# Optimization experiments

Hardware: AMD Instinct MI355X
Metric: run time of the kernel (lower is better)

The kernel has to match this reference:

```python
import jax, jax.numpy as jnp
import numpy as np

N = 32          # agents_num
IN_DIM = 16     # node feature dim (excluding 2 pos cols)
HID = 128
HEADS = 4
OUT = 5
DUEL_H = 256
RADIUS = 0.3
LATENT = HID + HID * HEADS * 2  # 1152
BS = 128


def _lin(k, i, o):
    s = 1.0 / np.sqrt(i)
    return jax.random.uniform(k, (i, o), minval=-s, maxval=s, dtype=jnp.float32)


def setup_inputs() -> dict:
    key = jax.random.key(0)
    ks = jax.random.split(key, 16)
    pos = jax.random.uniform(ks[0], (BS, N, 2))
    feats = jax.random.normal(ks[1], (BS, N, IN_DIM))
    aidx = jax.random.randint(ks[2], (BS,), 0, N).astype(jnp.float32)
    node = jnp.concatenate([pos, feats], axis=-1).reshape(BS, N * (2 + IN_DIM))
    obs = jnp.concatenate([node, aidx[:, None]], axis=1)  # (BS, N*(2+IN_DIM)+1)
    return {
        "obs": obs,
        "enc_w1": _lin(ks[3], IN_DIM, HID), "enc_b1": jnp.zeros((HID,)),
        "enc_w2": _lin(ks[4], HID, HID), "enc_b2": jnp.zeros((HID,)),
        "wl1": _lin(ks[5], HID, HEADS * HID), "wr1": _lin(ks[6], HID, HEADS * HID),
        "att1": jax.random.normal(ks[7], (HEADS, HID)) * 0.1, "bias1": jnp.zeros((HEADS * HID,)),
        "wl2": _lin(ks[8], HID * HEADS, HEADS * HID), "wr2": _lin(ks[9], HID * HEADS, HEADS * HID),
        "att2": jax.random.normal(ks[10], (HEADS, HID)) * 0.1, "bias2": jnp.zeros((HEADS * HID,)),
        "q_w1": _lin(ks[11], LATENT, DUEL_H), "q_b1": jnp.zeros((DUEL_H,)),
        "q_w2": _lin(ks[12], DUEL_H, OUT), "q_b2": jnp.zeros((OUT,)),
        "v_w1": _lin(ks[13], LATENT, DUEL_H), "v_b1": jnp.zeros((DUEL_H,)),
        "v_w2": _lin(ks[14], DUEL_H, 1), "v_b2": jnp.zeros((1,)),
    }


def _gatv2(x, adj, wl, wr, att, bias):
    # Dense-masked GATv2 (PyG semantics: lin_l on source j, lin_r on target i,
    # leaky_relu(x_i + x_j) . att, softmax over neighbors j, aggregate lin_l(x_j)).
    bs, n, _ = x.shape
    gl = (x @ wl).reshape(bs, n, HEADS, HID)  # source transform
    gr = (x @ wr).reshape(bs, n, HEADS, HID)  # target transform
    e = jax.nn.leaky_relu(gr[:, :, None] + gl[:, None, :], 0.2)  # [b, i, j, h, c]
    logits = jnp.einsum('bijhc,hc->bijh', e, att)
    logits = jnp.where(adj[..., None], logits, -jnp.inf)  # diag always True (self loops)
    alpha = jax.nn.softmax(logits, axis=2)
    out = jnp.einsum('bijh,bjhc->bihc', alpha, gl).reshape(bs, n, HEADS * HID)
    return out + bias


def reference(obs, enc_w1, enc_b1, enc_w2, enc_b2,
              wl1, wr1, att1, bias1, wl2, wr2, att2, bias2,
              q_w1, q_b1, q_w2, q_b2, v_w1, v_b1, v_w2, v_b2):
    bs = obs.shape[0]
    node = obs[:, :-1].reshape(bs, N, 2 + IN_DIM)
    pos, feats = node[..., :2], node[..., 2:]
    aidx = jnp.clip(obs[:, -1], 0, N - 1).astype(jnp.int32)

    # radius_graph (per-graph, loop=False) + GATv2 add_self_loops => diag True
    d2 = jnp.sum((pos[:, :, None] - pos[:, None, :]) ** 2, axis=-1)  # [bs, N, N]
    adj = (d2 < RADIUS ** 2) | jnp.eye(N, dtype=bool)

    # encoder MLP then ReLU (as in forward)
    h = jax.nn.relu(feats @ enc_w1 + enc_b1)
    x = jax.nn.relu(h @ enc_w2 + enc_b2)  # [bs, N, HID]

    b = jnp.arange(bs)
    x1 = x[b, aidx]  # [bs, HID]

    x = jax.nn.relu(_gatv2(x, adj, wl1, wr1, att1, bias1))  # [bs, N, HID*HEADS]
    x2 = x[b, aidx]

    x = jax.nn.relu(_gatv2(x, adj, wl2, wr2, att2, bias2))
    x3 = x[b, aidx]

    x_cat = jnp.concatenate([x1, x2, x3], axis=1)  # [bs, LATENT]

    q = jax.nn.relu(x_cat @ q_w1 + q_b1) @ q_w2 + q_b2  # [bs, OUT]
    v = jax.nn.relu(x_cat @ v_w1 + v_b1) @ v_w2 + v_b2  # [bs, 1]
    return q - q.mean(axis=1, keepdims=True) + v
```

## Files before the change

### kernel.cpp

```cpp
#include <hip/hip_runtime.h>
#include <hip/hip_bf16.h>

typedef unsigned int uint_t;
typedef unsigned short ushort_t;
typedef __attribute__((ext_vector_type(8))) short short8;
typedef __attribute__((ext_vector_type(4))) float floatx4;

__device__ __forceinline__ float4 fma4(float4 a, float s, float4 w){
  a.x += s*w.x; a.y += s*w.y; a.z += s*w.z; a.w += s*w.w; return a;
}
__device__ __forceinline__ float4 relu4(float4 a){
  return make_float4(fmaxf(a.x,0.f),fmaxf(a.y,0.f),fmaxf(a.z,0.f),fmaxf(a.w,0.f));
}
__device__ __forceinline__ unsigned bf16rne(float f){
  unsigned u = __float_as_uint(f);
  return (u + 0x7fffu + ((u>>16)&1u)) >> 16;
}
__device__ __forceinline__ uint_t packbf(float f){
  unsigned hb = bf16rne(f);
  float hf = __uint_as_float(hb<<16);
  unsigned lb = bf16rne(f - hf);
  return (hb<<16) | lb;
}
__device__ __forceinline__ uint4 pack4(float4 v){
  uint4 u; u.x=packbf(v.x); u.y=packbf(v.y); u.z=packbf(v.z); u.w=packbf(v.w); return u;
}
__device__ __forceinline__ float unpk(uint_t u){
  return __uint_as_float(u & 0xffff0000u) + __uint_as_float(u<<16);
}
#define UNPACK8(u0,u1,hi,lo) \
  hi[0]=(short)(u0.x>>16); lo[0]=(short)u0.x; \
  hi[1]=(short)(u0.y>>16); lo[1]=(short)u0.y; \
  hi[2]=(short)(u0.z>>16); lo[2]=(short)u0.z; \
  hi[3]=(short)(u0.w>>16); lo[3]=(short)u0.w; \
  hi[4]=(short)(u1.x>>16); lo[4]=(short)u1.x; \
  hi[5]=(short)(u1.y>>16); lo[5]=(short)u1.y; \
  hi[6]=(short)(u1.z>>16); lo[6]=(short)u1.z; \
  hi[7]=(short)(u1.w>>16); lo[7]=(short)u1.w;


__global__ __launch_bounds__(256) void prep_kernel(
    const float* __restrict__ obs,
    const float* __restrict__ enc_w1, const float* __restrict__ enc_b1,
    const float* __restrict__ enc_w2, const float* __restrict__ enc_b2,
    const float* __restrict__ wl1, const float* __restrict__ wr1,
    const float* __restrict__ wl2,
    const float* __restrict__ q_w1, const float* __restrict__ v_w1,
    ushort_t* __restrict__ wl1Thi, ushort_t* __restrict__ wl1Tlo,
    ushort_t* __restrict__ wr1Thi, ushort_t* __restrict__ wr1Tlo,
    ushort_t* __restrict__ wl2Thi, ushort_t* __restrict__ wl2Tlo,
    ushort_t* __restrict__ qw1Thi, ushort_t* __restrict__ qw1Tlo,
    ushort_t* __restrict__ vw1Thi, ushort_t* __restrict__ vw1Tlo,
    uint_t* __restrict__ xpk, uint_t* __restrict__ xcatpk,
    unsigned* __restrict__ adjw, int* __restrict__ aiw)
{
  const int t = threadIdx.x, bid = blockIdx.x;
  if (bid >= 512){
    __shared__ float sm[32][33];
    const int cw = bid - 512;
    const float* in; ushort_t* ohi; ushort_t* olo; int K, N, tt;
    if (cw < 64)        { in=wl1;  ohi=wl1Thi; olo=wl1Tlo; K=128;  N=512; tt=cw; }
    else if (cw < 128)  { in=wr1;  ohi=wr1Thi; olo=wr1Tlo; K=128;  N=512; tt=cw-64; }
    else if (cw < 384)  { in=wl2;  ohi=wl2Thi; olo=wl2Tlo; K=512;  N=512; tt=cw-128; }
    else if (cw < 672)  { in=q_w1; ohi=qw1Thi; olo=qw1Tlo; K=1152; N=256; tt=cw-384; }
    else                { in=v_w1; ohi=vw1Thi; olo=vw1Tlo; K=1152; N=256; tt=cw-672; }
    const int ktiles = K>>5;
    const int kt = tt % ktiles, nt = tt / ktiles;
    const int r = t>>5, c = t&31;
    #pragma unroll
    for (int i=0;i<4;i++)
      sm[r+i*8][c] = in[(size_t)(kt*32 + r + i*8)*N + nt*32 + c];
    __syncthreads();
    #pragma unroll
    for (int i=0;i<4;i++){
      const int nl = r + i*8;
      const int n  = nt*32 + nl;
      const float f = sm[c][nl];
      const unsigned hb = bf16rne(f);
      const float hf = __uint_as_float(hb<<16);
      const unsigned lb = bf16rne(f - hf);
      const size_t off = (size_t)(n>>4)*(16*K) + (size_t)kt*512 + (size_t)(n&15)*32 + c;
      ohi[off] = (ushort_t)hb;
      olo[off] = (ushort_t)lb;
    }
    return;
  }
  __shared__ float s_pos[64];
  __shared__ float s_feats[128];
  __shared__ __align__(16) float s_h[8*132];
  __shared__ int s_ai;
  const int s = bid>>2, g = bid&3;
  const float* ob = obs + s*577;

  if (t==0){
    float a = ob[576];
    a = fminf(fmaxf(a, 0.f), 31.f);
    s_ai = (int)a;
    if (g==0) aiw[s] = (int)a;
  }
  if (t < 128){ const int n=t>>4, f=t&15; s_feats[t] = ob[(g*8+n)*18+2+f]; }
  if (g==0 && t>=128 && t<192){ const int u=t-128; s_pos[u] = ob[(u>>1)*18 + (u&1)]; }
  __syncthreads();

  if (g==0 && t < 32){
    const float px = s_pos[2*t], py = s_pos[2*t+1];
    const float R2 = 0.09f;
    unsigned mm = 0u;
    for (int j=0;j<32;j++){
      const float dx = __fsub_rn(px, s_pos[2*j]), dy = __fsub_rn(py, s_pos[2*j+1]);
      const float d2 = __fadd_rn(__fmul_rn(dx,dx), __fmul_rn(dy,dy));
      if (d2 <= R2 || j==t) mm |= (1u<<j);
    }
    adjw[s*32+t] = mm;
  }

  const int n = t>>5, c0 = (t&31)*4;
  {
    float4 a = *(const float4*)(enc_b1+c0);
    #pragma unroll
    for (int f=0; f<16; f++)
      a = fma4(a, s_feats[n*16+f], *(const float4*)(enc_w1 + f*128 + c0));
    *(float4*)&s_h[n*132+c0] = relu4(a);
  }
  __syncthreads();
  {
    float4 a = *(const float4*)(enc_b2+c0);
    for (int k=0;k<128;k+=4){
      const float4 hv = *(const float4*)&s_h[n*132+k];
      a = fma4(a, hv.x, *(const float4*)(enc_w2 + (k+0)*128 + c0));
      a = fma4(a, hv.y, *(const float4*)(enc_w2 + (k+1)*128 + c0));
      a = fma4(a, hv.z, *(const float4*)(enc_w2 + (k+2)*128 + c0));
      a = fma4(a, hv.w, *(const float4*)(enc_w2 + (k+3)*128 + c0));
    }
    a = relu4(a);
    const uint4 p = pack4(a);
    const int i = g*8 + n;
    uint_t* xp = xpk + (size_t)(s*2 + (i>>4))*2048 + (c0>>5)*512 + (i&15)*32 + (c0&31);
    *(uint4*)xp = p;
    if (i == s_ai){
      uint_t* xc = xcatpk + (size_t)(s>>4)*18432 + (c0>>5)*512 + (s&15)*32 + (c0&31);
      *(uint4*)xc = p;
    }
  }
}

__global__ __launch_bounds__(512) void pa1_kernel(
    const uint_t* __restrict__ xpk,
    const ushort_t* __restrict__ wl1Thi, const ushort_t* __restrict__ wl1Tlo,
    const ushort_t* __restrict__ wr1Thi, const ushort_t* __restrict__ wr1Tlo,
    const float* __restrict__ att, const float* __restrict__ bias,
    const unsigned* __restrict__ adjw, const int* __restrict__ aiw,
    uint_t* __restrict__ x2pk, uint_t* __restrict__ xcatpk)
{
  __shared__ __align__(16) float s_gl[32*132];
  __shared__ __align__(16) float s_glB[32*132];
  __shared__ __align__(16) float s_gr[32*132];
  __shared__ __align__(16) float s_grB[32*132];
  __shared__ __align__(16) float s_att[128];
  __shared__ __align__(16) float s_b[128];
  __shared__ float s_lg[32*33];
  __shared__ unsigned s_adj[32];
  const int t = threadIdx.x;
  const int s = blockIdx.x >> 2, h = blockIdx.x & 3;
  const int w = t>>6, lane = t&63, m = lane&15, quad = lane>>4;
  const int ww = w&3, khalf = w>>2;

  if (t < 128){ s_att[t] = att[h*128 + t]; s_b[t] = bias[h*128 + t]; }
  if (t >= 224 && t < 256) s_adj[t-224] = adjw[s*32 + (t-224)];
  const int ai = aiw[s];

  const ushort_t* Bhi = (ww<2) ? wl1Thi : wr1Thi;
  const ushort_t* Blo = (ww<2) ? wl1Tlo : wr1Tlo;
  const int nbase = h*8 + (ww&1)*4;
  const int kcb = khalf*2;
  const uint_t* a0p = xpk + (size_t)(s*2+0)*2048 + m*32 + quad*8 + kcb*512;
  const uint_t* a1p = xpk + (size_t)(s*2+1)*2048 + m*32 + quad*8 + kcb*512;
  const ushort_t* bp0 = Bhi + (size_t)(nbase+0)*2048 + m*32 + quad*8 + kcb*512;
  const ushort_t* bp1 = Bhi + (size_t)(nbase+1)*2048 + m*32 + quad*8 + kcb*512;
  const ushort_t* bp2 = Bhi + (size_t)(nbase+2)*2048 + m*32 + quad*8 + kcb*512;
  const ushort_t* bp3 = Bhi + (size_t)(nbase+3)*2048 + m*32 + quad*8 + kcb*512;
  const size_t lod = (size_t)(Blo - Bhi);
  floatx4 acc[2][4];
  #pragma unroll
  for (int i=0;i<2;i++)
    #pragma unroll
    for (int j=0;j<4;j++) acc[i][j] = (floatx4){0.f,0.f,0.f,0.f};

  #pragma unroll
  for (int kc=0; kc<2; kc++){
    const uint4 u00 = *(const uint4*)(a0p + kc*512);
    const uint4 u01 = *(const uint4*)(a0p + kc*512 + 4);
    const uint4 u10 = *(const uint4*)(a1p + kc*512);
    const uint4 u11 = *(const uint4*)(a1p + kc*512 + 4);
    short8 ahi0, alo0, ahi1, alo1;
    UNPACK8(u00,u01,ahi0,alo0)
    UNPACK8(u10,u11,ahi1,alo1)
    const ushort_t* bps[4] = {bp0, bp1, bp2, bp3};
    #pragma unroll
    for (int nt=0; nt<4; nt++){
      const short8 bh = *(const short8*)(bps[nt] + kc*512);
      const short8 bl = *(const short8*)(bps[nt] + kc*512 + lod);
      acc[0][nt] = __builtin_amdgcn_mfma_f32_16x16x32_bf16(ahi0, bh, acc[0][nt], 0,0,0);
      acc[0][nt] = __builtin_amdgcn_mfma_f32_16x16x32_bf16(ahi0, bl, acc[0][nt], 0,0,0);
      acc[0][nt] = __builtin_amdgcn_mfma_f32_16x16x32_bf16(alo0, bh, acc[0][nt], 0,0,0);
      acc[1][nt] = __builtin_amdgcn_mfma_f32_16x16x32_bf16(ahi1, bh, acc[1][nt], 0,0,0);
      acc[1][nt] = __builtin_amdgcn_mfma_f32_16x16x32_bf16(ahi1, bl, acc[1][nt], 0,0,0);
      acc[1][nt] = __builtin_amdgcn_mfma_f32_16x16x32_bf16(alo1, bh, acc[1][nt], 0,0,0);
    }
  }
  {
    float* dst = (ww<2) ? (khalf ? s_glB : s_gl) : (khalf ? s_grB : s_gr);
    const int colbase = (ww&1)*64;
    #pragma unroll
    for (int nt=0; nt<4; nt++){
      const int col = colbase + nt*16 + m;
      #pragma unroll
      for (int r=0;r<4;r++){
        dst[(quad*4+r)*132 + col]      = acc[0][nt][r];
        dst[(16+quad*4+r)*132 + col]   = acc[1][nt][r];
      }
    }
  }
  __syncthreads();
  for (int e=t; e<32*132; e+=512){
    s_gl[e] += s_glB[e];
    s_gr[e] += s_grB[e];
  }
  __syncthreads();

  {
    const int i = t>>4, jb = t&15;
    float lacc[2] = {0.f,0.f};
    for (int c=0;c<128;c+=4){
      const float4 g = *(const float4*)&s_gr[i*132+c];
      const float4 a = *(const float4*)&s_att[c];
      #pragma unroll
      for (int mm=0;mm<2;mm++){
        const float4 gj = *(const float4*)&s_gl[(jb+16*mm)*132 + c];
        float ex = g.x+gj.x; ex = fmaxf(ex, 0.2f*ex);
        float ey = g.y+gj.y; ey = fmaxf(ey, 0.2f*ey);
        float ez = g.z+gj.z; ez = fmaxf(ez, 0.2f*ez);
        float ew = g.w+gj.w; ew = fmaxf(ew, 0.2f*ew);
        lacc[mm] += ex*a.x + ey*a.y + ez*a.z + ew*a.w;
      }
    }
    s_lg[i*33 + jb]      = lacc[0];
    s_lg[i*33 + jb + 16] = lacc[1];
  }
  __syncthreads();

  #pragma unroll
  for (int rnd=0; rnd<2; rnd++){
    const int i = rnd*16 + (t>>5), j = t&31;
    const float lg = s_lg[i*33+j];
    const bool ok = (s_adj[i]>>j)&1u;
    float v = ok ? lg : -3.0e38f;
    #pragma unroll
    for (int d_=16; d_; d_>>=1) v = fmaxf(v, __shfl_xor(v, d_, 32));
    const float e = ok ? __expf(lg - v) : 0.f;
    float sum = e;
    #pragma unroll
    for (int d_=16; d_; d_>>=1) sum += __shfl_xor(sum, d_, 32);
    s_lg[i*33+j] = e / sum;
  }
  __syncthreads();

  {
    const int i = t>>4, c0 = (t&15)*8;
    float4 o0 = make_float4(0.f,0.f,0.f,0.f), o1 = o0;
    for (int j=0;j<32;j++){
      const float al = s_lg[i*33+j];
      o0 = fma4(o0, al, *(const float4*)&s_gl[j*132 + c0]);
      o1 = fma4(o1, al, *(const float4*)&s_gl[j*132 + c0 + 4]);
    }
    const float4 b0 = *(const float4*)&s_b[c0];
    const float4 b1 = *(const float4*)&s_b[c0+4];
    o0 = relu4(make_float4(o0.x+b0.x, o0.y+b0.y, o0.z+b0.z, o0.w+b0.w));
    o1 = relu4(make_float4(o1.x+b1.x, o1.y+b1.y, o1.z+b1.z, o1.w+b1.w));
    const uint4 p0 = pack4(o0), p1 = pack4(o1);
    const int kb = h*128 + c0;
    uint_t* xp = x2pk + (size_t)(s*2 + (i>>4))*8192 + (kb>>5)*512 + (i&15)*32 + (kb&31);
    *(uint4*)&xp[0] = p0;
    *(uint4*)&xp[4] = p1;
    if (i == ai){
      const int kk = 128 + kb;
      uint_t* tp = xcatpk + (size_t)(s>>4)*18432 + (kk>>5)*512 + (s&15)*32 + (kk&31);
      *(uint4*)&tp[0] = p0;
      *(uint4*)&tp[4] = p1;
    }
  }
}

__global__ __launch_bounds__(512) void pa2_kernel(
    const uint_t* __restrict__ x2pk,
    const ushort_t* __restrict__ wl2Thi, const ushort_t* __restrict__ wl2Tlo,
    const float* __restrict__ wr2f,
    const float* __restrict__ att2, const float* __restrict__ bias2,
    const unsigned* __restrict__ adjw, const int* __restrict__ aiw,
    uint_t* __restrict__ xcatpk)
{
  __shared__ __align__(16) float s_gl[32*132];
  __shared__ __align__(16) float s_glB[32*132];
  __shared__ __align__(16) float s_xt[512];
  __shared__ __align__(16) float s_p2[4*128];
  __shared__ __align__(16) float s_at[128];
  __shared__ __align__(16) float s_bb[128];
  __shared__ float s_lg[32];
  __shared__ float s_al[32];
  const int t = threadIdx.x;
  const int s = blockIdx.x >> 2, h = blockIdx.x & 3;
  const int w = t>>6, lane = t&63, m = lane&15, quad = lane>>4;
  const int ww = w&3, khalf = w>>2;
  const int ai = aiw[s];
  const unsigned arow = adjw[s*32+ai];

  {
    const int kk = 128 + t;
    s_xt[t] = unpk(xcatpk[(size_t)(s>>4)*18432 + (kk>>5)*512 + (s&15)*32 + (kk&31)]);
  }
  if (t < 128){ s_at[t] = att2[h*128+t]; s_bb[t] = bias2[h*128+t]; }
  __syncthreads();

  {
    const int c = t&127, q4 = t>>7;
    const float* wp = wr2f + (size_t)(q4*128)*512 + h*128 + c;
    float ga = 0.f;
    #pragma unroll 8
    for (int k=0;k<128;k++) ga += s_xt[q4*128 + k] * wp[(size_t)k*512];
    s_p2[q4*128 + c] = ga;
  }

  const int kcb = khalf*8;
  const uint_t* a0p = x2pk + (size_t)(s*2+0)*8192 + m*32 + quad*8 + kcb*512;
  const uint_t* a1p = x2pk + (size_t)(s*2+1)*8192 + m*32 + quad*8 + kcb*512;
  const ushort_t* bq0 = wl2Thi + (size_t)(h*8 + ww*2+0)*8192 + m*32 + quad*8 + kcb*512;
  const ushort_t* bq1 = wl2Thi + (size_t)(h*8 + ww*2+1)*8192 + m*32 + quad*8 + kcb*512;
  const size_t lod = (size_t)(wl2Tlo - wl2Thi);
  floatx4 acc[2][2];
  #pragma unroll
  for (int i=0;i<2;i++){ acc[i][0] = (floatx4){0.f,0.f,0.f,0.f}; acc[i][1] = acc[i][0]; }
  #pragma unroll 4
  for (int kc=0; kc<8; kc++){
    const uint4 u00 = *(const uint4*)(a0p + kc*512);
    const uint4 u01 = *(const uint4*)(a0p + kc*512 + 4);
    const uint4 u10 = *(const uint4*)(a1p + kc*512);
    const uint4 u11 = *(const uint4*)(a1p + kc*512 + 4);
    short8 ahi0, alo0, ahi1, alo1;
    UNPACK8(u00,u01,ahi0,alo0)
    UNPACK8(u10,u11,ahi1,alo1)
    {
      const short8 bh = *(const short8*)(bq0 + kc*512);
      const short8 bl = *(const short8*)(bq0 + kc*512 + lod);
      acc[0][0] = __builtin_amdgcn_mfma_f32_16x16x32_bf16(ahi0, bh, acc[0][0], 0,0,0);
      acc[0][0] = __builtin_amdgcn_mfma_f32_16x16x32_bf16(ahi0, bl, acc[0][0], 0,0,0);
      acc[0][0] = __builtin_amdgcn_mfma_f32_16x16x32_bf16(alo0, bh, acc[0][0], 0,0,0);
      acc[1][0] = __builtin_amdgcn_mfma_f32_16x16x32_bf16(ahi1, bh, acc[1][0], 0,0,0);
      acc[1][0] = __builtin_amdgcn_mfma_f32_16x16x32_bf16(ahi1, bl, acc[1][0], 0,0,0);
      acc[1][0] = __builtin_amdgcn_mfma_f32_16x16x32_bf16(alo1, bh, acc[1][0], 0,0,0);
    }
    {
      const short8 bh = *(const short8*)(bq1 + kc*512);
      const short8 bl = *(const short8*)(bq1 + kc*512 + lod);
      acc[0][1] = __builtin_amdgcn_mfma_f32_16x16x32_bf16(ahi0, bh, acc[0][1], 0,0,0);
      acc[0][1] = __builtin_amdgcn_mfma_f32_16x16x32_bf16(ahi0, bl, acc[0][1], 0,0,0);
      acc[0][1] = __builtin_amdgcn_mfma_f32_16x16x32_bf16(alo0, bh, acc[0][1], 0,0,0);
      acc[1][1] = __builtin_amdgcn_mfma_f32_16x16x32_bf16(ahi1, bh, acc[1][1], 0,0,0);
      acc[1][1] = __builtin_amdgcn_mfma_f32_16x16x32_bf16(ahi1, bl, acc[1][1], 0,0,0);
      acc[1][1] = __builtin_amdgcn_mfma_f32_16x16x32_bf16(alo1, bh, acc[1][1], 0,0,0);
    }
  }
  {
    float* dst = khalf ? s_glB : s_gl;
    const int colbase = ww*32;
    #pragma unroll
    for (int nt=0; nt<2; nt++){
      const int col = colbase + nt*16 + m;
      #pragma unroll
      for (int r=0;r<4;r++){
        dst[(quad*4+r)*132 + col]    = acc[0][nt][r];
        dst[(16+quad*4+r)*132 + col] = acc[1][nt][r];
      }
    }
  }
  __syncthreads();
  for (int e=t; e<32*132; e+=512) s_gl[e] += s_glB[e];
  if (t < 128) s_p2[t] = s_p2[t] + s_p2[128+t] + s_p2[256+t] + s_p2[384+t];
  __syncthreads();

  if (t < 256){
    const int j = t>>3, p = t&7;
    float sum = 0.f;
    #pragma unroll
    for (int q=0;q<4;q++){
      const int c = p*16 + q*4;
      const float4 g = *(const float4*)&s_gl[j*132 + c];
      const float4 r = *(const float4*)&s_p2[c];
      const float4 a = *(const float4*)&s_at[c];
      float e0 = r.x+g.x; e0 = fmaxf(e0, 0.2f*e0);
      float e1 = r.y+g.y; e1 = fmaxf(e1, 0.2f*e1);
      float e2 = r.z+g.z; e2 = fmaxf(e2, 0.2f*e2);
      float e3 = r.w+g.w; e3 = fmaxf(e3, 0.2f*e3);
      sum += e0*a.x + e1*a.y + e2*a.z + e3*a.w;
    }
    sum += __shfl_xor(sum,1,64);
    sum += __shfl_xor(sum,2,64);
    sum += __shfl_xor(sum,4,64);
    if (p==0) s_lg[j] = sum;
  }
  __syncthreads();
  if (t < 32){
    const float lg = s_lg[t];
    const bool ok = (arow>>t)&1u;
    float v = ok ? lg : -3.0e38f;
    #pragma unroll
    for (int d_=16; d_; d_>>=1) v = fmaxf(v, __shfl_xor(v, d_, 32));
    const float e = ok ? __expf(lg - v) : 0.f;
    float sm = e;
    #pragma unroll
    for (int d_=16; d_; d_>>=1) sm += __shfl_xor(sm, d_, 32);
    s_al[t] = e / sm;
  }
  __syncthreads();
  if (t < 128){
    float acc2 = 0.f;
    #pragma unroll 8
    for (int j=0;j<32;j++) acc2 += s_al[j] * s_gl[j*132 + t];
    const int kk = 640 + h*128 + t;
    xcatpk[(size_t)(s>>4)*18432 + (kk>>5)*512 + (s&15)*32 + (kk&31)]
        = packbf(fmaxf(acc2 + s_bb[t], 0.f));
  }
}

template<int KD>
__global__ __launch_bounds__(256) void mfma_gemm(
    const uint_t* __restrict__ A1, int rbs1,
    const ushort_t* __restrict__ B0hi, const ushort_t* __restrict__ B0lo,
    const ushort_t* __restrict__ B1hi, const ushort_t* __restrict__ B1lo,
    float* __restrict__ C0, float* __restrict__ C1,
    int nct1, int ctsplit)
{
  const int t = threadIdx.x;
  const int w = t>>6, lane = t&63;
  const int m = lane & 15, quad = lane >> 4;
  const int bid = blockIdx.x;
  const int rt = bid / nct1, ct = bid % nct1;
  const ushort_t* Bhi; const ushort_t* Blo; float* C; int cb;
  if (ct < ctsplit){ Bhi = B0hi; Blo = B0lo; C = C0; cb = ct*64; }
  else             { Bhi = B1hi; Blo = B1lo; C = C1; cb = (ct-ctsplit)*64; }
  const uint_t* ap = A1 + (size_t)(rt*4 + w)*rbs1 + m*32 + quad*8;
  const ushort_t* bp0 = Bhi + (size_t)((cb>>4)+0)*(16*KD) + m*32 + quad*8;
  const ushort_t* bp1 = Bhi + (size_t)((cb>>4)+1)*(16*KD) + m*32 + quad*8;
  const ushort_t* bp2 = Bhi + (size_t)((cb>>4)+2)*(16*KD) + m*32 + quad*8;
  const ushort_t* bp3 = Bhi + (size_t)((cb>>4)+3)*(16*KD) + m*32 + quad*8;
  const size_t lod = (size_t)(Blo - Bhi);
  floatx4 acc[4];
  #pragma unroll
  for (int i=0;i<4;i++) acc[i] = (floatx4){0.f,0.f,0.f,0.f};

  for (int kc=0; kc<KD/32; kc++){
    const uint4 ua0 = *(const uint4*)(ap);
    const uint4 ua1 = *(const uint4*)(ap+4);
    ap += 512;
    short8 ahi, alo;
    UNPACK8(ua0,ua1,ahi,alo)
    {
      const short8 bh = *(const short8*)(bp0);
      const short8 bl = *(const short8*)(bp0 + lod);
      acc[0] = __builtin_amdgcn_mfma_f32_16x16x32_bf16(ahi, bh, acc[0], 0,0,0);
      acc[0] = __builtin_amdgcn_mfma_f32_16x16x32_bf16(ahi, bl, acc[0], 0,0,0);
      acc[0] = __builtin_amdgcn_mfma_f32_16x16x32_bf16(alo, bh, acc[0], 0,0,0);
      bp0 += 512;
    }
    {
      const short8 bh = *(const short8*)(bp1);
      const short8 bl = *(const short8*)(bp1 + lod);
      acc[1] = __builtin_amdgcn_mfma_f32_16x16x32_bf16(ahi, bh, acc[1], 0,0,0);
      acc[1] = __builtin_amdgcn_mfma_f32_16x16x32_bf16(ahi, bl, acc[1], 0,0,0);
      acc[1] = __builtin_amdgcn_mfma_f32_16x16x32_bf16(alo, bh, acc[1], 0,0,0);
      bp1 += 512;
    }
    {
      const short8 bh = *(const short8*)(bp2);
      const short8 bl = *(const short8*)(bp2 + lod);
      acc[2] = __builtin_amdgcn_mfma_f32_16x16x32_bf16(ahi, bh, acc[2], 0,0,0);
      acc[2] = __builtin_amdgcn_mfma_f32_16x16x32_bf16(ahi, bl, acc[2], 0,0,0);
      acc[2] = __builtin_amdgcn_mfma_f32_16x16x32_bf16(alo, bh, acc[2], 0,0,0);
      bp2 += 512;
    }
    {
      const short8 bh = *(const short8*)(bp3);
      const short8 bl = *(const short8*)(bp3 + lod);
      acc[3] = __builtin_amdgcn_mfma_f32_16x16x32_bf16(ahi, bh, acc[3], 0,0,0);
      acc[3] = __builtin_amdgcn_mfma_f32_16x16x32_bf16(ahi, bl, acc[3], 0,0,0);
      acc[3] = __builtin_amdgcn_mfma_f32_16x16x32_bf16(alo, bh, acc[3], 0,0,0);
      bp3 += 512;
    }
  }
  const int crow0 = rt*64 + w*16 + quad*4;
  #pragma unroll
  for (int nt2=0; nt2<4; nt2++){
    const int col = cb + nt2*16 + m;
    #pragma unroll
    for (int r=0;r<4;r++)
      C[(size_t)(crow0 + r)*512 + col] = acc[nt2][r];
  }
}

__global__ __launch_bounds__(256) void heads2_kernel(
    const float* __restrict__ Ch,
    const float* __restrict__ q_b1, const float* __restrict__ q_w2, const float* __restrict__ q_b2,
    const float* __restrict__ v_b1, const float* __restrict__ v_w2, const float* __restrict__ v_b2,
    float* __restrict__ out)
{
  __shared__ float s_p[4*6];
  const int t = threadIdx.x, s = blockIdx.x;
  const float hq = fmaxf(Ch[(size_t)s*512 + t]       + q_b1[t], 0.f);
  const float hv = fmaxf(Ch[(size_t)s*512 + 256 + t] + v_b1[t], 0.f);
  float p[6];
  #pragma unroll
  for (int o=0;o<5;o++) p[o] = hq * q_w2[t*5+o];
  p[5] = hv * v_w2[t];
  #pragma unroll
  for (int d_=32; d_; d_>>=1){
    #pragma unroll
    for (int o=0;o<6;o++) p[o] += __shfl_xor(p[o], d_, 64);
  }
  const int w = t>>6, lane = t&63;
  if (lane==0){
    #pragma unroll
    for (int o=0;o<6;o++) s_p[w*6+o] = p[o];
  }
  __syncthreads();
  if (t < 6) s_p[t] = s_p[t] + s_p[6+t] + s_p[12+t] + s_p[18+t];
  __syncthreads();
  if (t < 5){
    const float q0 = s_p[0]+q_b2[0], q1 = s_p[1]+q_b2[1], q2 = s_p[2]+q_b2[2],
                q3 = s_p[3]+q_b2[3], q4 = s_p[4]+q_b2[4];
    const float mean = (q0+q1+q2+q3+q4) / 5.0f;
    const float v = s_p[5] + v_b2[0];
    const float qt = (t==0?q0:t==1?q1:t==2?q2:t==3?q3:q4);
    out[s*5+t] = qt - mean + v;
  }
}

extern "C" void kernel_launch(void* const* d_in, const int* in_sizes, int n_in,
                              void* d_out, int out_size, void* d_ws, size_t ws_size,
                              hipStream_t stream) {
  (void)n_in; (void)out_size; (void)ws_size;
  const float* obs    = (const float*)d_in[0];
  const float* enc_w1 = (const float*)d_in[1];
  const float* enc_b1 = (const float*)d_in[2];
  const float* enc_w2 = (const float*)d_in[3];
  const float* enc_b2 = (const float*)d_in[4];
  const float* wl1    = (const float*)d_in[5];
  const float* wr1    = (const float*)d_in[6];
  const float* att1   = (const float*)d_in[7];
  const float* bias1  = (const float*)d_in[8];
  const float* wl2    = (const float*)d_in[9];
  const float* wr2    = (const float*)d_in[10];
  const float* att2   = (const float*)d_in[11];
  const float* bias2  = (const float*)d_in[12];
  const float* q_w1   = (const float*)d_in[13];
  const float* q_b1   = (const float*)d_in[14];
  const float* q_w2   = (const float*)d_in[15];
  const float* q_b2   = (const float*)d_in[16];
  const float* v_w1   = (const float*)d_in[17];
  const float* v_b1   = (const float*)d_in[18];
  const float* v_w2   = (const float*)d_in[19];
  const float* v_b2   = (const float*)d_in[20];

  char* ws = (char*)d_ws;
  uint_t*   x_pk    = (uint_t*)  (ws + 0);
  uint_t*   xcat_pk = (uint_t*)  (ws + 2097152);
  unsigned* adjw    = (unsigned*)(ws + 2686976);
  int*      aiw     = (int*)     (ws + 2703360);
  uint_t*   x2_pk   = (uint_t*)  (ws + 2703872);
  ushort_t* wl1Thi  = (ushort_t*)(ws + 11092480);
  ushort_t* wl1Tlo  = (ushort_t*)(ws + 11223552);
  ushort_t* wr1Thi  = (ushort_t*)(ws + 11354624);
  ushort_t* wr1Tlo  = (ushort_t*)(ws + 11485696);
  ushort_t* wl2Thi  = (ushort_t*)(ws + 11616768);
  ushort_t* wl2Tlo  = (ushort_t*)(ws + 12141056);
  ushort_t* qw1Thi  = (ushort_t*)(ws + 12665344);
  ushort_t* qw1Tlo  = (ushort_t*)(ws + 13255168);
  ushort_t* vw1Thi  = (ushort_t*)(ws + 13844992);
  ushort_t* vw1Tlo  = (ushort_t*)(ws + 14434816);
  float*    headsC  = (float*)   (ws + 15024640);

  const int bs = in_sizes[0] / 577;

  prep_kernel<<<512 + 960, 256, 0, stream>>>(obs, enc_w1, enc_b1, enc_w2, enc_b2,
      wl1, wr1, wl2, q_w1, v_w1,
      wl1Thi, wl1Tlo, wr1Thi, wr1Tlo, wl2Thi, wl2Tlo,
      qw1Thi, qw1Tlo, vw1Thi, vw1Tlo,
      x_pk, xcat_pk, adjw, aiw);

  pa1_kernel<<<bs*4, 512, 0, stream>>>(x_pk, wl1Thi, wl1Tlo, wr1Thi, wr1Tlo,
                                       att1, bias1, adjw, aiw, x2_pk, xcat_pk);

  pa2_kernel<<<bs*4, 512, 0, stream>>>(x2_pk, wl2Thi, wl2Tlo, wr2,
                                       att2, bias2, adjw, aiw, xcat_pk);

  mfma_gemm<1152><<<16, 256, 0, stream>>>(xcat_pk, 18432,
      qw1Thi, qw1Tlo, vw1Thi, vw1Tlo, headsC, headsC + 256, 8, 4);

  heads2_kernel<<<bs, 256, 0, stream>>>(headsC, q_b1, q_w2, q_b2, v_b1, v_w2, v_b2,
                                        (float*)d_out);
}
```

Before: 191.8 us.

## Move weight conversions into pa1 and fuse head GEMM with head epilogue

Result: slower. 211.8 us (+10.4%).

```diff
diff --git a/kernel.cpp b/kernel.cpp
--- a/kernel.cpp
+++ b/kernel.cpp
@@ -44,13 +44,8 @@
     const float* __restrict__ enc_w1, const float* __restrict__ enc_b1,
     const float* __restrict__ enc_w2, const float* __restrict__ enc_b2,
     const float* __restrict__ wl1, const float* __restrict__ wr1,
-    const float* __restrict__ wl2,
-    const float* __restrict__ q_w1, const float* __restrict__ v_w1,
     ushort_t* __restrict__ wl1Thi, ushort_t* __restrict__ wl1Tlo,
     ushort_t* __restrict__ wr1Thi, ushort_t* __restrict__ wr1Tlo,
-    ushort_t* __restrict__ wl2Thi, ushort_t* __restrict__ wl2Tlo,
-    ushort_t* __restrict__ qw1Thi, ushort_t* __restrict__ qw1Tlo,
-    ushort_t* __restrict__ vw1Thi, ushort_t* __restrict__ vw1Tlo,
     uint_t* __restrict__ xpk, uint_t* __restrict__ xcatpk,
     unsigned* __restrict__ adjw, int* __restrict__ aiw)
 {
@@ -58,12 +53,10 @@
   if (bid >= 512){
     __shared__ float sm[32][33];
     const int cw = bid - 512;
-    const float* in; ushort_t* ohi; ushort_t* olo; int K, N, tt;
-    if (cw < 64)        { in=wl1;  ohi=wl1Thi; olo=wl1Tlo; K=128;  N=512; tt=cw; }
-    else if (cw < 128)  { in=wr1;  ohi=wr1Thi; olo=wr1Tlo; K=128;  N=512; tt=cw-64; }
-    else if (cw < 384)  { in=wl2;  ohi=wl2Thi; olo=wl2Tlo; K=512;  N=512; tt=cw-128; }
-    else if (cw < 672)  { in=q_w1; ohi=qw1Thi; olo=qw1Tlo; K=1152; N=256; tt=cw-384; }
-    else                { in=v_w1; ohi=vw1Thi; olo=vw1Tlo; K=1152; N=256; tt=cw-672; }
+    const float* in; ushort_t* ohi; ushort_t* olo; int tt;
+    const int K = 128, N = 512;
+    if (cw < 64){ in=wl1; ohi=wl1Thi; olo=wl1Tlo; tt=cw; }
+    else        { in=wr1; ohi=wr1Thi; olo=wr1Tlo; tt=cw-64; }
     const int ktiles = K>>5;
     const int kt = tt % ktiles, nt = tt / ktiles;
     const int r = t>>5, c = t&31;
@@ -150,6 +143,10 @@
     const ushort_t* __restrict__ wr1Thi, const ushort_t* __restrict__ wr1Tlo,
     const float* __restrict__ att, const float* __restrict__ bias,
     const unsigned* __restrict__ adjw, const int* __restrict__ aiw,
+    const float* __restrict__ wl2, const float* __restrict__ q_w1, const float* __restrict__ v_w1,
+    ushort_t* __restrict__ wl2Thi, ushort_t* __restrict__ wl2Tlo,
+    ushort_t* __restrict__ qw1Thi, ushort_t* __restrict__ qw1Tlo,
+    ushort_t* __restrict__ vw1Thi, ushort_t* __restrict__ vw1Tlo,
     uint_t* __restrict__ x2pk, uint_t* __restrict__ xcatpk)
 {
   __shared__ __align__(16) float s_gl[32*132];
@@ -160,8 +157,37 @@
   __shared__ __align__(16) float s_b[128];
   __shared__ float s_lg[32*33];
   __shared__ unsigned s_adj[32];
-  const int t = threadIdx.x;
-  const int s = blockIdx.x >> 2, h = blockIdx.x & 3;
+  const int t = threadIdx.x, bid = blockIdx.x;
+
+  if (bid >= 512){
+    const int cw = bid - 512;
+    const float* in; ushort_t* ohi; ushort_t* olo; int K, N, tt;
+    if (cw < 256)      { in=wl2;  ohi=wl2Thi; olo=wl2Tlo; K=512;  N=512; tt=cw; }
+    else if (cw < 544) { in=q_w1; ohi=qw1Thi; olo=qw1Tlo; K=1152; N=256; tt=cw-256; }
+    else               { in=v_w1; ohi=vw1Thi; olo=vw1Tlo; K=1152; N=256; tt=cw-544; }
+    const int ktiles = K>>5;
+    const int kt = tt % ktiles, nt = tt / ktiles;
+    const int r = t>>5, c = t&31;
+    #pragma unroll
+    for (int i=0;i<2;i++)
+      s_gl[(r+i*16)*33 + c] = in[(size_t)(kt*32 + r + i*16)*N + nt*32 + c];
+    __syncthreads();
+    #pragma unroll
+    for (int i=0;i<2;i++){
+      const int nl = r + i*16;
+      const int n  = nt*32 + nl;
+      const float f = s_gl[c*33 + nl];
+      const unsigned hb = bf16rne(f);
+      const float hf = __uint_as_float(hb<<16);
+      const unsigned lb = bf16rne(f - hf);
+      const size_t off = (size_t)(n>>4)*(16*K) + (size_t)kt*512 + (size_t)(n&15)*32 + c;
+      ohi[off] = (ushort_t)hb;
+      olo[off] = (ushort_t)lb;
+    }
+    return;
+  }
+
+  const int s = bid >> 2, h = bid & 3;
   const int w = t>>6, lane = t&63, m = lane&15, quad = lane>>4;
   const int ww = w&3, khalf = w>>2;
 
@@ -388,11 +414,11 @@
   __syncthreads();
 
   if (t < 256){
-    const int j = t>>3, p = t&7;
+    const int j = t>>3, pq = t&7;
     float sum = 0.f;
     #pragma unroll
     for (int q=0;q<4;q++){
-      const int c = p*16 + q*4;
+      const int c = pq*16 + q*4;
       const float4 g = *(const float4*)&s_gl[j*132 + c];
       const float4 r = *(const float4*)&s_p2[c];
       const float4 a = *(const float4*)&s_at[c];
@@ -405,7 +431,7 @@
     sum += __shfl_xor(sum,1,64);
     sum += __shfl_xor(sum,2,64);
     sum += __shfl_xor(sum,4,64);
-    if (p==0) s_lg[j] = sum;
+    if (pq==0) s_lg[j] = sum;
   }
   __syncthreads();
   if (t < 32){
@@ -431,115 +457,87 @@
   }
 }
 
-template<int KD>
-__global__ __launch_bounds__(256) void mfma_gemm(
-    const uint_t* __restrict__ A1, int rbs1,
-    const ushort_t* __restrict__ B0hi, const ushort_t* __restrict__ B0lo,
-    const ushort_t* __restrict__ B1hi, const ushort_t* __restrict__ B1lo,
-    float* __restrict__ C0, float* __restrict__ C1,
-    int nct1, int ctsplit)
+__global__ __launch_bounds__(512) void heads_kernel(
+    const uint_t* __restrict__ xcatpk,
+    const ushort_t* __restrict__ qw1Thi, const ushort_t* __restrict__ qw1Tlo,
+    const ushort_t* __restrict__ vw1Thi, const ushort_t* __restrict__ vw1Tlo,
+    const float* __restrict__ q_b1, const float* __restrict__ q_w2, const float* __restrict__ q_b2,
+    const float* __restrict__ v_b1, const float* __restrict__ v_w2, const float* __restrict__ v_b2,
+    float* __restrict__ out)
 {
-  const int t = threadIdx.x;
-  const int w = t>>6, lane = t&63;
-  const int m = lane & 15, quad = lane >> 4;
-  const int bid = blockIdx.x;
-  const int rt = bid / nct1, ct = bid % nct1;
-  const ushort_t* Bhi; const ushort_t* Blo; float* C; int cb;
-  if (ct < ctsplit){ Bhi = B0hi; Blo = B0lo; C = C0; cb = ct*64; }
-  else             { Bhi = B1hi; Blo = B1lo; C = C1; cb = (ct-ctsplit)*64; }
-  const uint_t* ap = A1 + (size_t)(rt*4 + w)*rbs1 + m*32 + quad*8;
-  const ushort_t* bp0 = Bhi + (size_t)((cb>>4)+0)*(16*KD) + m*32 + quad*8;
-  const ushort_t* bp1 = Bhi + (size_t)((cb>>4)+1)*(16*KD) + m*32 + quad*8;
-  const ushort_t* bp2 = Bhi + (size_t)((cb>>4)+2)*(16*KD) + m*32 + quad*8;
-  const ushort_t* bp3 = Bhi + (size_t)((cb>>4)+3)*(16*KD) + m*32 + quad*8;
-  const size_t lod = (size_t)(Blo - Bhi);
+  __shared__ __align__(16) float s_C[16*520];
+  const int t = threadIdx.x, rt = blockIdx.x;
+  const int w = t>>6, lane = t&63, m = lane&15, quad = lane>>4;
+
+  const size_t lod = (size_t)(qw1Tlo - qw1Thi);
+  const uint_t* ap = xcatpk + (size_t)rt*18432 + m*32 + quad*8;
+  const ushort_t* bps[4];
+  #pragma unroll
+  for (int nt=0; nt<4; nt++){
+    const int ntg = w*4 + nt;
+    const ushort_t* Bhi = (ntg < 16) ? qw1Thi : vw1Thi;
+    const int cbrow = (ntg < 16) ? ntg : (ntg - 16);
+    bps[nt] = Bhi + (size_t)cbrow*18432 + m*32 + quad*8;
+  }
   floatx4 acc[4];
   #pragma unroll
   for (int i=0;i<4;i++) acc[i] = (floatx4){0.f,0.f,0.f,0.f};
-
-  for (int kc=0; kc<KD/32; kc++){
+  for (int kc=0; kc<36; kc++){
     const uint4 ua0 = *(const uint4*)(ap);
     const uint4 ua1 = *(const uint4*)(ap+4);
     ap += 512;
     short8 ahi, alo;
     UNPACK8(ua0,ua1,ahi,alo)
-    {
-      const short8 bh = *(const short8*)(bp0);
-      const short8 bl = *(const short8*)(bp0 + lod);
-      acc[0] = __builtin_amdgcn_mfma_f32_16x16x32_bf16(ahi, bh, acc[0], 0,0,0);
-      acc[0] = __builtin_amdgcn_mfma_f32_16x16x32_bf16(ahi, bl, acc[0], 0,0,0);
-      acc[0] = __builtin_amdgcn_mfma_f32_16x16x32_bf16(alo, bh, acc[0], 0,0,0);
-      bp0 += 512;
-    }
-    {
-      const short8 bh = *(const short8*)(bp1);
-      const short8 bl = *(const short8*)(bp1 + lod);
-      acc[1] = __builtin_amdgcn_mfma_f32_16x16x32_bf16(ahi, bh, acc[1], 0,0,0);
-      acc[1] = __builtin_amdgcn_mfma_f32_16x16x32_bf16(ahi, bl, acc[1], 0,0,0);
-      acc[1] = __builtin_amdgcn_mfma_f32_16x16x32_bf16(alo, bh, acc[1], 0,0,0);
-      bp1 += 512;
-    }
-    {
-      const short8 bh = *(const short8*)(bp2);
-      const short8 bl = *(const short8*)(bp2 + lod);
-      acc[2] = __builtin_amdgcn_mfma_f32_16x16x32_bf16(ahi, bh, acc[2], 0,0,0);
-      acc[2] = __builtin_amdgcn_mfma_f32_16x16x32_bf16(ahi, bl, acc[2], 0,0,0);
-      acc[2] = __builtin_amdgcn_mfma_f32_16x16x32_bf16(alo, bh, acc[2], 0,0,0);
-      bp2 += 512;
-    }
-    {
-      const short8 bh = *(const short8*)(bp3);
-      const short8 bl = *(const short8*)(bp3 + lod);
-      acc[3] = __builtin_amdgcn_mfma_f32_16x16x32_bf16(ahi, bh, acc[3], 0,0,0);
-      acc[3] = __builtin_amdgcn_mfma_f32_16x16x32_bf16(ahi, bl, acc[3], 0,0,0);
-      acc[3] = __builtin_amdgcn_mfma_f32_16x16x32_bf16(alo, bh, acc[3], 0,0,0);
-      bp3 += 512;
-    }
-  }
-  const int crow0 = rt*64 + w*16 + quad*4;
+    #pragma unroll
+    for (int nt=0; nt<4; nt++){
+      const short8 bh = *(const short8*)(bps[nt]);
+      const short8 bl = *(const short8*)(bps[nt] + lod);
+      acc[nt] = __builtin_amdgcn_mfma_f32_16x16x32_bf16(ahi, bh, acc[nt], 0,0,0);
+      acc[nt] = __builtin_amdgcn_mfma_f32_16x16x32_bf16(ahi, bl, acc[nt], 0,0,0);
+      acc[nt] = __builtin_amdgcn_mfma_f32_16x16x32_bf16(alo, bh, acc[nt], 0,0,0);
+      bps[nt] += 512;
+    }
+  }
   #pragma unroll
-  for (int nt2=0; nt2<4; nt2++){
-    const int col = cb + nt2*16 + m;
+  for (int nt=0; nt<4; nt++){
+    const int colg = (w*4 + nt)*16 + m;
     #pragma unroll
     for (int r=0;r<4;r++)
-      C[(size_t)(crow0 + r)*512 + col] = acc[nt2][r];
-  }
-}
-
-__global__ __launch_bounds__(256) void heads2_kernel(
-    const float* __restrict__ Ch,
-    const float* __restrict__ q_b1, const float* __restrict__ q_w2, const float* __restrict__ q_b2,
-    const float* __restrict__ v_b1, const float* __restrict__ v_w2, const float* __restrict__ v_b2,
-    float* __restrict__ out)
-{
-  __shared__ float s_p[4*6];
-  const int t = threadIdx.x, s = blockIdx.x;
-  const float hq = fmaxf(Ch[(size_t)s*512 + t]       + q_b1[t], 0.f);
-  const float hv = fmaxf(Ch[(size_t)s*512 + 256 + t] + v_b1[t], 0.f);
-  float p[6];
-  #pragma unroll
-  for (int o=0;o<5;o++) p[o] = hq * q_w2[t*5+o];
-  p[5] = hv * v_w2[t];
-  #pragma unroll
-  for (int d_=32; d_; d_>>=1){
-    #pragma unroll
-    for (int o=0;o<6;o++) p[o] += __shfl_xor(p[o], d_, 64);
-  }
-  const int w = t>>6, lane = t&63;
-  if (lane==0){
-    #pragma unroll
-    for (int o=0;o<6;o++) s_p[w*6+o] = p[o];
-  }
-  __syncthreads();
-  if (t < 6) s_p[t] = s_p[t] + s_p[6+t] + s_p[12+t] + s_p[18+t];
-  __syncthreads();
-  if (t < 5){
-    const float q0 = s_p[0]+q_b2[0], q1 = s_p[1]+q_b2[1], q2 = s_p[2]+q_b2[2],
-                q3 = s_p[3]+q_b2[3], q4 = s_p[4]+q_b2[4];
-    const float mean = (q0+q1+q2+q3+q4) / 5.0f;
-    const float v = s_p[5] + v_b2[0];
-    const float qt = (t==0?q0:t==1?q1:t==2?q2:t==3?q3:q4);
-    out[s*5+t] = qt - mean + v;
+      s_C[(quad*4+r)*520 + colg] = acc[nt][r];
+  }
+  __syncthreads();
+
+  {
+    const int s16 = t>>5, j = t&31;
+    float pq[5] = {0.f,0.f,0.f,0.f,0.f};
+    float pv = 0.f;
+    #pragma unroll
+    for (int cc=0; cc<8; cc++){
+      const int c = j*8 + cc;
+      const float hq = fmaxf(s_C[s16*520 + c]       + q_b1[c], 0.f);
+      const float hv = fmaxf(s_C[s16*520 + 256 + c] + v_b1[c], 0.f);
+      #pragma unroll
+      for (int o=0;o<5;o++) pq[o] += hq * q_w2[c*5+o];
+      pv += hv * v_w2[c];
+    }
+    #pragma unroll
+    for (int d_=16; d_; d_>>=1){
+      #pragma unroll
+      for (int o=0;o<5;o++) pq[o] += __shfl_xor(pq[o], d_, 32);
+      pv += __shfl_xor(pv, d_, 32);
+    }
+    if (j == 0){
+      const float q0 = pq[0]+q_b2[0], q1 = pq[1]+q_b2[1], q2 = pq[2]+q_b2[2],
+                  q3 = pq[3]+q_b2[3], q4 = pq[4]+q_b2[4];
+      const float mean = (q0+q1+q2+q3+q4) / 5.0f;
+      const float v = pv + v_b2[0];
+      const int s = rt*16 + s16;
+      out[s*5+0] = q0 - mean + v;
+      out[s*5+1] = q1 - mean + v;
+      out[s*5+2] = q2 - mean + v;
+      out[s*5+3] = q3 - mean + v;
+      out[s*5+4] = q4 - mean + v;
+    }
   }
 }
 
@@ -585,25 +583,22 @@
   ushort_t* qw1Tlo  = (ushort_t*)(ws + 13255168);
   ushort_t* vw1Thi  = (ushort_t*)(ws + 13844992);
   ushort_t* vw1Tlo  = (ushort_t*)(ws + 14434816);
-  float*    headsC  = (float*)   (ws + 15024640);
 
   const int bs = in_sizes[0] / 577;
 
-  prep_kernel<<<512 + 960, 256, 0, stream>>>(obs, enc_w1, enc_b1, enc_w2, enc_b2,
-      wl1, wr1, wl2, q_w1, v_w1,
-      wl1Thi, wl1Tlo, wr1Thi, wr1Tlo, wl2Thi, wl2Tlo,
-      qw1Thi, qw1Tlo, vw1Thi, vw1Tlo,
+  prep_kernel<<<512 + 128, 256, 0, stream>>>(obs, enc_w1, enc_b1, enc_w2, enc_b2,
+      wl1, wr1, wl1Thi, wl1Tlo, wr1Thi, wr1Tlo,
       x_pk, xcat_pk, adjw, aiw);
 
-  pa1_kernel<<<bs*4, 512, 0, stream>>>(x_pk, wl1Thi, wl1Tlo, wr1Thi, wr1Tlo,
-                                       att1, bias1, adjw, aiw, x2_pk, xcat_pk);
+  pa1_kernel<<<512 + 832, 512, 0, stream>>>(x_pk, wl1Thi, wl1Tlo, wr1Thi, wr1Tlo,
+      att1, bias1, adjw, aiw,
+      wl2, q_w1, v_w1, wl2Thi, wl2Tlo, qw1Thi, qw1Tlo, vw1Thi, vw1Tlo,
+      x2_pk, xcat_pk);
 
   pa2_kernel<<<bs*4, 512, 0, stream>>>(x2_pk, wl2Thi, wl2Tlo, wr2,
                                        att2, bias2, adjw, aiw, xcat_pk);
 
-  mfma_gemm<1152><<<16, 256, 0, stream>>>(xcat_pk, 18432,
-      qw1Thi, qw1Tlo, vw1Thi, vw1Tlo, headsC, headsC + 256, 8, 4);
-
-  heads2_kernel<<<bs, 256, 0, stream>>>(headsC, q_b1, q_w2, q_b2, v_b1, v_w2, v_b2,
-                                        (float*)d_out);
-}
+  heads_kernel<<<8, 512, 0, stream>>>(xcat_pk, qw1Thi, qw1Tlo, vw1Thi, vw1Tlo,
+                                      q_b1, q_w2, q_b2, v_b1, v_w2, v_b2,
+                                      (float*)d_out);
+}
```
